# Performance work log

Hardware: AMD Instinct MI355X
Metric: run time of the kernel (lower is better)

## Reference

```python
import jax, jax.numpy as jnp
import numpy as np
from jax.ops import segment_sum

N_NODES = 100000
N_EDGES = 1600000
HIDDEN = 64
N_LAYERS = 4
N_CLASSES = 10
N_GRAPHS = 512


def setup_inputs() -> dict:
    key = jax.random.key(0)
    ks = jax.random.split(key, 9)
    x = jax.random.normal(ks[0], (N_NODES, HIDDEN), dtype=jnp.float32)
    edge_index = jax.random.randint(ks[1], (2, N_EDGES), 0, N_NODES, dtype=jnp.int32)
    batch = jnp.sort(jax.random.randint(ks[2], (N_NODES,), 0, N_GRAPHS, dtype=jnp.int32))
    s = 0.05
    W_enc = jax.random.normal(ks[3], (HIDDEN, HIDDEN), dtype=jnp.float32) * s
    b_enc = jax.random.normal(ks[4], (HIDDEN,), dtype=jnp.float32) * s
    W_conv = jax.random.normal(ks[5], (N_LAYERS, HIDDEN, HIDDEN), dtype=jnp.float32) * s
    b_conv = jax.random.normal(ks[6], (N_LAYERS, HIDDEN), dtype=jnp.float32) * s
    W_out = jax.random.normal(ks[7], (HIDDEN, N_CLASSES), dtype=jnp.float32) * s
    b_out = jax.random.normal(ks[8], (N_CLASSES,), dtype=jnp.float32) * s
    return {"x": x, "edge_index": edge_index, "batch": batch,
            "W_enc": W_enc, "b_enc": b_enc, "W_conv": W_conv, "b_conv": b_conv,
            "W_out": W_out, "b_out": b_out, "num_graphs": N_GRAPHS}


def reference(x, edge_index, batch, W_enc, b_enc, W_conv, b_conv, W_out, b_out, num_graphs):
    N = x.shape[0]
    src, dst = edge_index[0], edge_index[1]
    # atom_encoder: Linear
    h = x @ W_enc + b_enc
    # GCN symmetric normalization with self-loops (PyG GCNConv default):
    # deg counts incoming edges (dst) plus the self-loop.
    deg = segment_sum(jnp.ones_like(src, dtype=h.dtype), dst, num_segments=N) + 1.0
    deg_inv_sqrt = jax.lax.rsqrt(deg)
    deg_inv = 1.0 / deg  # self-loop norm = d^-1/2 * d^-1/2
    edge_norm = (deg_inv_sqrt[src] * deg_inv_sqrt[dst])[:, None]  # [E,1]
    for l in range(W_conv.shape[0]):
        hl = h @ W_conv[l]                          # [N,H]
        msg = hl[src] * edge_norm                   # gather + normalize [E,H]
        agg = segment_sum(msg, dst, num_segments=N) # scatter-add
        h = agg + hl * deg_inv[:, None] + b_conv[l] # self-loop + bias
        h = jax.nn.silu(h)                          # dropout p=0 / eval: identity
    # global_add_pool over graph ids
    pooled = segment_sum(h, batch, num_segments=num_graphs)  # [G,H]
    # readout: Linear + ReLU (make_mlp with hidden_layers=1)
    out = jax.nn.relu(pooled @ W_out + b_out)
    return out
```

## Files before the change

kernel.cpp:

```cpp
#include <hip/hip_runtime.h>
#include <math.h>

#define HIDDEN 64
#define N_LAYERS 4
#define N_CLASSES 10
#define N_GRAPHS 512
#define BSH 8
#define NPB 256
#define PART_K 2048

typedef _Float16 __h;
typedef __attribute__((ext_vector_type(4))) _Float16 half4;
typedef __attribute__((ext_vector_type(8))) _Float16 half8;
typedef __attribute__((ext_vector_type(4))) float f32x4;

__global__ __launch_bounds__(256) void k_histA(const int* __restrict__ dst,
                                               int* __restrict__ ghist, int E, int NB) {
    __shared__ int hist[512];
    int t = threadIdx.x;
    hist[t] = 0; hist[t + 256] = 0;
    __syncthreads();
    int base = blockIdx.x * PART_K;
    int kend = min(PART_K, E - base);
    for (int k = t; k < kend; k += 256) atomicAdd(&hist[dst[base + k] >> BSH], 1);
    __syncthreads();
    for (int j = t; j < NB; j += 256) {
        int h = hist[j];
        if (h) atomicAdd(&ghist[j], h);
    }
}

__global__ __launch_bounds__(256) void k_bucketscan(const int* __restrict__ ghist,
                                                    int* __restrict__ bucketbase,
                                                    int* __restrict__ gcur, int NB) {
    __shared__ int s[256];
    int t = threadIdx.x;
    int j0 = 2 * t, j1 = 2 * t + 1;
    int h0 = (j0 < NB) ? ghist[j0] : 0;
    int h1 = (j1 < NB) ? ghist[j1] : 0;
    s[t] = h0 + h1; __syncthreads();
    for (int o = 1; o < 256; o <<= 1) {
        int x = (t >= o) ? s[t - o] : 0;
        __syncthreads();
        s[t] += x;
        __syncthreads();
    }
    int base = (t == 0) ? 0 : s[t - 1];
    if (j0 <= NB) { bucketbase[j0] = base;      gcur[j0] = base; }
    if (j1 <= NB) { bucketbase[j1] = base + h0; gcur[j1] = base + h0; }
}

__global__ __launch_bounds__(256) void k_partition(const int* __restrict__ src,
                                                   const int* __restrict__ dst,
                                                   int* __restrict__ gcur,
                                                   int* __restrict__ packed,
                                                   int E, int NB) {
    __shared__ int hist[512];
    __shared__ int scanE[512];
    __shared__ int cur[512];
    __shared__ int delta[512];
    __shared__ int ps[256];
    __shared__ int stage[PART_K];
    __shared__ unsigned short stgj[PART_K];
    int t = threadIdx.x;
    int base = blockIdx.x * PART_K;
    int kend = min(PART_K, E - base);

    hist[t] = 0; hist[t + 256] = 0;
    __syncthreads();
    for (int k = t; k < kend; k += 256) atomicAdd(&hist[dst[base + k] >> BSH], 1);
    __syncthreads();

    int j0 = 2 * t, j1 = j0 + 1;
    int h0 = hist[j0], h1 = hist[j1];
    ps[t] = h0 + h1; __syncthreads();
    for (int o = 1; o < 256; o <<= 1) {
        int x = (t >= o) ? ps[t - o] : 0;
        __syncthreads();
        ps[t] += x;
        __syncthreads();
    }
    int bexc = (t == 0) ? 0 : ps[t - 1];
    scanE[j0] = bexc;
    scanE[j1] = bexc + h0;
    __syncthreads();

    for (int j = t; j < NB; j += 256) {
        int h = hist[j];
        int g = h ? atomicAdd(&gcur[j], h) : 0;
        delta[j] = g - scanE[j];
        cur[j]   = scanE[j];
    }
    __syncthreads();

    for (int k = t; k < kend; k += 256) {
        int d = dst[base + k], s = src[base + k];
        int j = d >> BSH;
        int pos = atomicAdd(&cur[j], 1);
        stage[pos] = (s << BSH) | (d & (NPB - 1));
        stgj[pos]  = (unsigned short)j;
    }
    __syncthreads();

    for (int i = t; i < kend; i += 256) {
        packed[i + delta[stgj[i]]] = stage[i];
    }
}

__global__ __launch_bounds__(256) void k_fill3(const int* __restrict__ packed,
                                               const int* __restrict__ bucketbase,
                                               int* __restrict__ rowptr,
                                               float* __restrict__ dis,
                                               int* __restrict__ csr_src,
                                               int N, int E) {
    __shared__ int cnt[256];
    __shared__ int rp[256];
    int j = blockIdx.x;
    int t = threadIdx.x;
    int node0 = j << BSH;
    int segb = bucketbase[j];
    int sege = bucketbase[j + 1];

    cnt[t] = 0; __syncthreads();
    for (int i = segb + t; i < sege; i += 256) atomicAdd(&cnt[packed[i] & (NPB - 1)], 1);
    __syncthreads();

    int c = cnt[t];
    rp[t] = c; __syncthreads();
    for (int o = 1; o < 256; o <<= 1) {
        int x = (t >= o) ? rp[t - o] : 0;
        __syncthreads();
        rp[t] += x;
        __syncthreads();
    }
    int node = node0 + t;
    int start = segb + rp[t] - c + node;
    if (node < N) {
        rowptr[node] = start;
        dis[node] = rsqrtf((float)c + 1.0f);
        csr_src[start] = node;
        if (node == N - 1) rowptr[N] = E + N;
    }
    __syncthreads();
    cnt[t] = start + 1;
    __syncthreads();
    for (int i = segb + t; i < sege; i += 256) {
        int v = packed[i];
        int slot = atomicAdd(&cnt[v & (NPB - 1)], 1);
        csr_src[slot] = v >> BSH;
    }
}

__device__ __forceinline__ half4 shfl_xor_h4(half4 v, int m) {
    uint2 u = __builtin_bit_cast(uint2, v);
    u.x = __shfl_xor((int)u.x, m);
    u.y = __shfl_xor((int)u.y, m);
    return __builtin_bit_cast(half4, u);
}

__global__ __launch_bounds__(256) void k_prepW(const float* __restrict__ Wconv,
                                               const float* __restrict__ Wenc,
                                               __h* __restrict__ Wh) {
    int idx = blockIdx.x * 256 + threadIdx.x;
    int l = idx >> 12;
    int kn = idx & 4095;
    int k = kn >> 6, n = kn & 63;
    int nt = n >> 4, nl = n & 15;
    int kt = k >> 5, kr = k & 31;
    int quad = kr >> 3, j = kr & 7;
    int lane = quad * 16 + nl;
    int pos = (((nt * 2 + kt) * 64 + lane) << 3) + j;
    float w = (l < N_LAYERS) ? Wconv[(size_t)l * 4096 + kn] : Wenc[kn];
    Wh[(l << 12) + pos] = (__h)w;
}

__global__ __launch_bounds__(256) void k_layer(const int* __restrict__ csr_src,
                                               const int* __restrict__ rowptr,
                                               const float* __restrict__ dis,
                                               const __h* __restrict__ G,
                                               const __h* __restrict__ Wh,
                                               const float* __restrict__ bias,
                                               const int* __restrict__ batch,
                                               __h* __restrict__ Gho,
                                               float* __restrict__ pooled,
                                               int N, int last) {
    __shared__ __attribute__((aligned(16))) __h At[4][16][72];
    int wave = threadIdx.x >> 6;
    int lane = threadIdx.x & 63;
    int row0 = (blockIdx.x * 4 + wave) * 16;
    if (row0 >= N) return;
    int grp = lane >> 4;
    int f4  = lane & 15;

    int rpi = row0 + lane;
    int rpv = rowptr[rpi > N ? N : rpi];

    const half4 z = {(__h)0.f, (__h)0.f, (__h)0.f, (__h)0.f};
    for (int i = 0; i < 16; ++i) {
        int beg = __shfl(rpv, i);
        int end = __shfl(rpv, i + 1);
        half4 a = z;
        int e = beg + grp;
        while (e < end) {
            int s0 = csr_src[e];
            int s1 = (e + 4  < end) ? csr_src[e + 4]  : -1;
            int s2 = (e + 8  < end) ? csr_src[e + 8]  : -1;
            int s3 = (e + 12 < end) ? csr_src[e + 12] : -1;
            int s4 = (e + 16 < end) ? csr_src[e + 16] : -1;
            int s5 = (e + 20 < end) ? csr_src[e + 20] : -1;
            int s6 = (e + 24 < end) ? csr_src[e + 24] : -1;
            int s7 = (e + 28 < end) ? csr_src[e + 28] : -1;
            half4 r0 = ((const half4*)(G + (size_t)s0 * 64))[f4];
            half4 r1 = (s1 >= 0) ? ((const half4*)(G + (size_t)s1 * 64))[f4] : z;
            half4 r2 = (s2 >= 0) ? ((const half4*)(G + (size_t)s2 * 64))[f4] : z;
            half4 r3 = (s3 >= 0) ? ((const half4*)(G + (size_t)s3 * 64))[f4] : z;
            half4 r4 = (s4 >= 0) ? ((const half4*)(G + (size_t)s4 * 64))[f4] : z;
            half4 r5 = (s5 >= 0) ? ((const half4*)(G + (size_t)s5 * 64))[f4] : z;
            half4 r6 = (s6 >= 0) ? ((const half4*)(G + (size_t)s6 * 64))[f4] : z;
            half4 r7 = (s7 >= 0) ? ((const half4*)(G + (size_t)s7 * 64))[f4] : z;
            a += r0; a += r1; a += r2; a += r3;
            a += r4; a += r5; a += r6; a += r7;
            e += 32;
        }
        a += shfl_xor_h4(a, 16);
        a += shfl_xor_h4(a, 32);
        if (grp == 0) {
            int node = row0 + i;
            float df = (node < N) ? dis[node] : 0.0f;
            __h dd = (__h)df;
            ((half4*)&At[wave][i][0])[f4] = a * dd;
        }
    }

    int quad = grp, nl = f4;
    half8 bf[4][2];
    #pragma unroll
    for (int nt = 0; nt < 4; ++nt)
        #pragma unroll
        for (int kt = 0; kt < 2; ++kt)
            bf[nt][kt] = *(const half8*)(Wh + (((nt * 2 + kt) * 64 + lane) << 3));

    half8 a0 = *(const half8*)&At[wave][nl][quad * 8];
    half8 a1 = *(const half8*)&At[wave][nl][32 + quad * 8];

    f32x4 acc[4];
    #pragma unroll
    for (int nt = 0; nt < 4; ++nt) {
        acc[nt] = (f32x4){0.f, 0.f, 0.f, 0.f};
        acc[nt] = __builtin_amdgcn_mfma_f32_16x16x32_f16(a0, bf[nt][0], acc[nt], 0, 0, 0);
        acc[nt] = __builtin_amdgcn_mfma_f32_16x16x32_f16(a1, bf[nt][1], acc[nt], 0, 0, 0);
    }

    float b[4];
    #pragma unroll
    for (int nt = 0; nt < 4; ++nt) b[nt] = bias[nt * 16 + nl];

    if (!last) {
        #pragma unroll
        for (int reg = 0; reg < 4; ++reg) {
            int rr = row0 + quad * 4 + reg;
            if (rr < N) {
                float ds_ = dis[rr];
                #pragma unroll
                for (int nt = 0; nt < 4; ++nt) {
                    float v = acc[nt][reg] + b[nt];
                    v = v / (1.0f + expf(-v));
                    Gho[(size_t)rr * 64 + nt * 16 + nl] = (__h)(ds_ * v);
                }
            }
        }
    } else {
        float run[4] = {0.f, 0.f, 0.f, 0.f};
        int cur = -1;
        #pragma unroll
        for (int reg = 0; reg < 4; ++reg) {
            int rr = row0 + quad * 4 + reg;
            if (rr < N) {
                int bi = batch[rr];
                float vals[4];
                #pragma unroll
                for (int nt = 0; nt < 4; ++nt) {
                    float v = acc[nt][reg] + b[nt];
                    vals[nt] = v / (1.0f + expf(-v));
                }
                if (bi != cur) {
                    if (cur >= 0) {
                        #pragma unroll
                        for (int nt = 0; nt < 4; ++nt)
                            atomicAdd(&pooled[cur * 64 + nt * 16 + nl], run[nt]);
                    }
                    cur = bi;
                    #pragma unroll
                    for (int nt = 0; nt < 4; ++nt) run[nt] = vals[nt];
                } else {
                    #pragma unroll
                    for (int nt = 0; nt < 4; ++nt) run[nt] += vals[nt];
                }
            }
        }
        if (cur >= 0) {
            #pragma unroll
            for (int nt = 0; nt < 4; ++nt)
                atomicAdd(&pooled[cur * 64 + nt * 16 + nl], run[nt]);
        }
    }
}

__global__ __launch_bounds__(256) void k_gemm_mfma(const float* __restrict__ xf,
                                                   const __h* __restrict__ Wh,
                                                   const float* __restrict__ bias,
                                                   const float* __restrict__ dis,
                                                   __h* __restrict__ Gho,
                                                   int N) {
    int wave = threadIdx.x >> 6;
    int lane = threadIdx.x & 63;
    int row0 = (blockIdx.x * 4 + wave) * 32;
    if (row0 >= N) return;
    int quad = lane >> 4, nl = lane & 15;

    half8 bf[4][2];
    #pragma unroll
    for (int nt = 0; nt < 4; ++nt)
        #pragma unroll
        for (int kt = 0; kt < 2; ++kt)
            bf[nt][kt] = *(const half8*)(Wh + (((nt * 2 + kt) * 64 + lane) << 3));

    f32x4 acc[2][4];
    #pragma unroll
    for (int h = 0; h < 2; ++h) {
        int r = row0 + h * 16 + nl; if (r >= N) r = N - 1;
        const float* ap = xf + (size_t)r * 64 + quad * 8;
        float4 v0 = ((const float4*)ap)[0];
        float4 v1 = ((const float4*)ap)[1];
        float4 v2 = ((const float4*)(ap + 32))[0];
        float4 v3 = ((const float4*)(ap + 32))[1];
        half8 a0 = (half8){(__h)v0.x, (__h)v0.y, (__h)v0.z, (__h)v0.w,
                           (__h)v1.x, (__h)v1.y, (__h)v1.z, (__h)v1.w};
        half8 a1 = (half8){(__h)v2.x, (__h)v2.y, (__h)v2.z, (__h)v2.w,
                           (__h)v3.x, (__h)v3.y, (__h)v3.z, (__h)v3.w};
        #pragma unroll
        for (int nt = 0; nt < 4; ++nt) {
            acc[h][nt] = (f32x4){0.f, 0.f, 0.f, 0.f};
            acc[h][nt] = __builtin_amdgcn_mfma_f32_16x16x32_f16(a0, bf[nt][0], acc[h][nt], 0, 0, 0);
            acc[h][nt] = __builtin_amdgcn_mfma_f32_16x16x32_f16(a1, bf[nt][1], acc[h][nt], 0, 0, 0);
        }
    }

    float b[4];
    #pragma unroll
    for (int nt = 0; nt < 4; ++nt) b[nt] = bias[nt * 16 + nl];

    #pragma unroll
    for (int h = 0; h < 2; ++h) {
        #pragma unroll
        for (int reg = 0; reg < 4; ++reg) {
            int rr = row0 + h * 16 + quad * 4 + reg;
            if (rr < N) {
                float ds = dis[rr];
                #pragma unroll
                for (int nt = 0; nt < 4; ++nt) {
                    float v = acc[h][nt][reg] + b[nt];
                    Gho[(size_t)rr * 64 + nt * 16 + nl] = (__h)(ds * v);
                }
            }
        }
    }
}

__global__ __launch_bounds__(256) void k_readout(const float* __restrict__ pooled,
                                                 const float* __restrict__ Wout,
                                                 const float* __restrict__ bout,
                                                 float* __restrict__ out) {
    int idx = blockIdx.x * 256 + threadIdx.x;
    if (idx >= N_GRAPHS * N_CLASSES) return;
    int g = idx / N_CLASSES, c = idx % N_CLASSES;
    float s = bout[c];
    #pragma unroll
    for (int j = 0; j < 64; ++j) s += pooled[g * 64 + j] * Wout[j * N_CLASSES + c];
    out[idx] = fmaxf(s, 0.0f);
}

extern "C" void kernel_launch(void* const* d_in, const int* in_sizes, int n_in,
                              void* d_out, int out_size, void* d_ws, size_t ws_size,
                              hipStream_t stream) {
    const float* x      = (const float*)d_in[0];
    const int*   ei     = (const int*)d_in[1];
    const int*   batch  = (const int*)d_in[2];
    const float* W_enc  = (const float*)d_in[3];
    const float* b_enc  = (const float*)d_in[4];
    const float* W_conv = (const float*)d_in[5];
    const float* b_conv = (const float*)d_in[6];
    const float* W_out  = (const float*)d_in[7];
    const float* b_out  = (const float*)d_in[8];
    float* out = (float*)d_out;

    const int N = in_sizes[2];
    const int E = in_sizes[1] / 2;
    const int* src = ei;
    const int* dst = ei + E;
    const int NB   = (N + NPB - 1) >> BSH;
    const int NBLK = (E + PART_K - 1) / PART_K;

    char* ws = (char*)d_ws;
    size_t off = 0;
    auto alloc = [&](size_t bytes) -> char* {
        char* p = ws + off;
        off += (bytes + 255) & ~(size_t)255;
        return p;
    };
    int*   ghist      = (int*)alloc((size_t)(NB + 1) * sizeof(int));
    int*   bucketbase = (int*)alloc((size_t)(NB + 1) * sizeof(int));
    int*   gcur       = (int*)alloc((size_t)(NB + 1) * sizeof(int));
    int*   packed     = (int*)alloc((size_t)E * sizeof(int));
    int*   csr_src    = (int*)alloc((size_t)(E + N) * sizeof(int));
    int*   rowptr     = (int*)alloc((size_t)(N + 1) * sizeof(int));
    float* dis        = (float*)alloc((size_t)N * sizeof(float));
    __h*   bufA       = (__h*)alloc((size_t)N * HIDDEN * sizeof(__h));
    __h*   bufB       = (__h*)alloc((size_t)N * HIDDEN * sizeof(__h));
    __h*   Wh         = (__h*)alloc((size_t)(N_LAYERS + 1) * 4096 * sizeof(__h));
    float* pooled     = (float*)alloc((size_t)N_GRAPHS * HIDDEN * sizeof(float));
    (void)ws_size;

    hipMemsetAsync(ghist, 0, (size_t)(NB + 1) * sizeof(int), stream);
    hipMemsetAsync(pooled, 0, (size_t)N_GRAPHS * HIDDEN * sizeof(float), stream);

    k_histA     <<<NBLK, 256, 0, stream>>>(dst, ghist, E, NB);
    k_bucketscan<<<1,    256, 0, stream>>>(ghist, bucketbase, gcur, NB);
    k_partition <<<NBLK, 256, 0, stream>>>(src, dst, gcur, packed, E, NB);
    k_fill3     <<<NB,   256, 0, stream>>>(packed, bucketbase, rowptr, dis, csr_src, N, E);
    k_prepW<<<((N_LAYERS + 1) * 4096) / 256, 256, 0, stream>>>(W_conv, W_enc, Wh);

    int gb32 = (N + 127) / 128;
    k_gemm_mfma<<<gb32, 256, 0, stream>>>(x, Wh + (size_t)N_LAYERS * 4096, b_enc,
                                          dis, bufA, N);

    __h* bufs[2] = {bufA, bufB};
    int glayer = (N + 63) / 64;
    for (int l = 0; l < N_LAYERS; ++l) {
        int last = (l == N_LAYERS - 1);
        k_layer<<<glayer, 256, 0, stream>>>(csr_src, rowptr, dis, bufs[l & 1],
                                            Wh + (size_t)l * 4096,
                                            b_conv + (size_t)l * HIDDEN, batch,
                                            bufs[(l + 1) & 1], pooled, N, last);
    }

    k_readout<<<(N_GRAPHS * N_CLASSES + 255) / 256, 256, 0, stream>>>(pooled, W_out, b_out, out);
}
```

Baseline: 336.8 us.

## Split each 16-row tile across two waves and stage CSR indices in LDS

The layer kernel now gives each 16-row tile to two waves, each aggregating 8 rows, so a block covers 32 rows and twice as many blocks are launched. The tile's CSR source indices are loaded cooperatively and coalesced into shared memory before the gather, with a fallback to global memory past a 512-entry cap. Both waves compute the MFMA redundantly and each writes back only its half. The aim is more parallelism on the latency-bound gather and cheaper index loads, at the cost of two block barriers, duplicated MFMA work and extra shared memory.

```diff
diff --git a/kernel.cpp b/kernel.cpp
--- a/kernel.cpp
+++ b/kernel.cpp
@@ -8,6 +8,7 @@
 #define BSH 8
 #define NPB 256
 #define PART_K 2048
+#define IDX_CAP 512
 
 typedef _Float16 __h;
 typedef __attribute__((ext_vector_type(4))) _Float16 half4;
@@ -184,32 +185,47 @@
                                                __h* __restrict__ Gho,
                                                float* __restrict__ pooled,
                                                int N, int last) {
-    __shared__ __attribute__((aligned(16))) __h At[4][16][72];
-    int wave = threadIdx.x >> 6;
-    int lane = threadIdx.x & 63;
-    int row0 = (blockIdx.x * 4 + wave) * 16;
-    if (row0 >= N) return;
+    __shared__ __attribute__((aligned(16))) __h At[2][16][72];
+    __shared__ int sidx[2][IDX_CAP];
+    int tid  = threadIdx.x;
+    int wave = tid >> 6;
+    int lane = tid & 63;
+    int tile = wave >> 1;
+    int half = wave & 1;
+    int trow0 = blockIdx.x * 32 + tile * 16;
     int grp = lane >> 4;
     int f4  = lane & 15;
 
-    int rpi = row0 + lane;
+    int rpi = trow0 + lane;
     int rpv = rowptr[rpi > N ? N : rpi];
+    int beg0 = __shfl(rpv, 0);
+    int endL = __shfl(rpv, 16);
+    int Lc   = endL - beg0; if (Lc > IDX_CAP) Lc = IDX_CAP;
+
+    int t2 = tid & 127;
+    const int* __restrict__ gsrc = csr_src + beg0;
+    for (int k = t2; k < Lc; k += 128) sidx[tile][k] = gsrc[k];
+    __syncthreads();
 
     const half4 z = {(__h)0.f, (__h)0.f, (__h)0.f, (__h)0.f};
-    for (int i = 0; i < 16; ++i) {
+    const int* sp = sidx[tile];
+    #pragma unroll 2
+    for (int r = 0; r < 8; ++r) {
+        int i = half * 8 + r;
         int beg = __shfl(rpv, i);
         int end = __shfl(rpv, i + 1);
         half4 a = z;
         int e = beg + grp;
         while (e < end) {
-            int s0 = csr_src[e];
-            int s1 = (e + 4  < end) ? csr_src[e + 4]  : -1;
-            int s2 = (e + 8  < end) ? csr_src[e + 8]  : -1;
-            int s3 = (e + 12 < end) ? csr_src[e + 12] : -1;
-            int s4 = (e + 16 < end) ? csr_src[e + 16] : -1;
-            int s5 = (e + 20 < end) ? csr_src[e + 20] : -1;
-            int s6 = (e + 24 < end) ? csr_src[e + 24] : -1;
-            int s7 = (e + 28 < end) ? csr_src[e + 28] : -1;
+            int o = e - beg0;
+            int s0 =                  (o      < IDX_CAP) ? sp[o]      : csr_src[e];
+            int s1 = (e + 4  < end) ? ((o + 4  < IDX_CAP) ? sp[o + 4]  : csr_src[e + 4])  : -1;
+            int s2 = (e + 8  < end) ? ((o + 8  < IDX_CAP) ? sp[o + 8]  : csr_src[e + 8])  : -1;
+            int s3 = (e + 12 < end) ? ((o + 12 < IDX_CAP) ? sp[o + 12] : csr_src[e + 12]) : -1;
+            int s4 = (e + 16 < end) ? ((o + 16 < IDX_CAP) ? sp[o + 16] : csr_src[e + 16]) : -1;
+            int s5 = (e + 20 < end) ? ((o + 20 < IDX_CAP) ? sp[o + 20] : csr_src[e + 20]) : -1;
+            int s6 = (e + 24 < end) ? ((o + 24 < IDX_CAP) ? sp[o + 24] : csr_src[e + 24]) : -1;
+            int s7 = (e + 28 < end) ? ((o + 28 < IDX_CAP) ? sp[o + 28] : csr_src[e + 28]) : -1;
             half4 r0 = ((const half4*)(G + (size_t)s0 * 64))[f4];
             half4 r1 = (s1 >= 0) ? ((const half4*)(G + (size_t)s1 * 64))[f4] : z;
             half4 r2 = (s2 >= 0) ? ((const half4*)(G + (size_t)s2 * 64))[f4] : z;
@@ -225,12 +241,13 @@
         a += shfl_xor_h4(a, 16);
         a += shfl_xor_h4(a, 32);
         if (grp == 0) {
-            int node = row0 + i;
+            int node = trow0 + i;
             float df = (node < N) ? dis[node] : 0.0f;
             __h dd = (__h)df;
-            ((half4*)&At[wave][i][0])[f4] = a * dd;
-        }
-    }
+            ((half4*)&At[tile][i][0])[f4] = a * dd;
+        }
+    }
+    __syncthreads();
 
     int quad = grp, nl = f4;
     half8 bf[4][2];
@@ -240,8 +257,8 @@
         for (int kt = 0; kt < 2; ++kt)
             bf[nt][kt] = *(const half8*)(Wh + (((nt * 2 + kt) * 64 + lane) << 3));
 
-    half8 a0 = *(const half8*)&At[wave][nl][quad * 8];
-    half8 a1 = *(const half8*)&At[wave][nl][32 + quad * 8];
+    half8 a0 = *(const half8*)&At[tile][nl][quad * 8];
+    half8 a1 = *(const half8*)&At[tile][nl][32 + quad * 8];
 
     f32x4 acc[4];
     #pragma unroll
@@ -255,53 +272,59 @@
     #pragma unroll
     for (int nt = 0; nt < 4; ++nt) b[nt] = bias[nt * 16 + nl];
 
+    bool own = ((quad >> 1) == half);
+
     if (!last) {
-        #pragma unroll
-        for (int reg = 0; reg < 4; ++reg) {
-            int rr = row0 + quad * 4 + reg;
-            if (rr < N) {
-                float ds_ = dis[rr];
-                #pragma unroll
-                for (int nt = 0; nt < 4; ++nt) {
-                    float v = acc[nt][reg] + b[nt];
-                    v = v / (1.0f + expf(-v));
-                    Gho[(size_t)rr * 64 + nt * 16 + nl] = (__h)(ds_ * v);
+        if (own) {
+            #pragma unroll
+            for (int reg = 0; reg < 4; ++reg) {
+                int rr = trow0 + quad * 4 + reg;
+                if (rr < N) {
+                    float ds_ = dis[rr];
+                    #pragma unroll
+                    for (int nt = 0; nt < 4; ++nt) {
+                        float v = acc[nt][reg] + b[nt];
+                        v = v / (1.0f + expf(-v));
+                        Gho[(size_t)rr * 64 + nt * 16 + nl] = (__h)(ds_ * v);
+                    }
                 }
             }
         }
     } else {
-        float run[4] = {0.f, 0.f, 0.f, 0.f};
-        int cur = -1;
-        #pragma unroll
-        for (int reg = 0; reg < 4; ++reg) {
-            int rr = row0 + quad * 4 + reg;
-            if (rr < N) {
-                int bi = batch[rr];
-                float vals[4];
-                #pragma unroll
-                for (int nt = 0; nt < 4; ++nt) {
-                    float v = acc[nt][reg] + b[nt];
-                    vals[nt] = v / (1.0f + expf(-v));
-                }
-                if (bi != cur) {
-                    if (cur >= 0) {
+        if (own) {
+            float run[4] = {0.f, 0.f, 0.f, 0.f};
+            int cur = -1;
+            #pragma unroll
+            for (int reg = 0; reg < 4; ++reg) {
+                int rr = trow0 + quad * 4 + reg;
+                if (rr < N) {
+                    int bi = batch[rr];
+                    float vals[4];
+                    #pragma unroll
+                    for (int nt = 0; nt < 4; ++nt) {
+                        float v = acc[nt][reg] + b[nt];
+                        vals[nt] = v / (1.0f + expf(-v));
+                    }
+                    if (bi != cur) {
+                        if (cur >= 0) {
+                            #pragma unroll
+                            for (int nt = 0; nt < 4; ++nt)
+                                atomicAdd(&pooled[cur * 64 + nt * 16 + nl], run[nt]);
+                        }
+                        cur = bi;
                         #pragma unroll
-                        for (int nt = 0; nt < 4; ++nt)
-                            atomicAdd(&pooled[cur * 64 + nt * 16 + nl], run[nt]);
+                        for (int nt = 0; nt < 4; ++nt) run[nt] = vals[nt];
+                    } else {
+                        #pragma unroll
+                        for (int nt = 0; nt < 4; ++nt) run[nt] += vals[nt];
                     }
-                    cur = bi;
-                    #pragma unroll
-                    for (int nt = 0; nt < 4; ++nt) run[nt] = vals[nt];
-                } else {
-                    #pragma unroll
-                    for (int nt = 0; nt < 4; ++nt) run[nt] += vals[nt];
                 }
             }
-        }
-        if (cur >= 0) {
-            #pragma unroll
-            for (int nt = 0; nt < 4; ++nt)
-                atomicAdd(&pooled[cur * 64 + nt * 16 + nl], run[nt]);
+            if (cur >= 0) {
+                #pragma unroll
+                for (int nt = 0; nt < 4; ++nt)
+                    atomicAdd(&pooled[cur * 64 + nt * 16 + nl], run[nt]);
+            }
         }
     }
 }
@@ -435,7 +458,7 @@
                                           dis, bufA, N);
 
     __h* bufs[2] = {bufA, bufB};
-    int glayer = (N + 63) / 64;
+    int glayer = (N + 31) / 32;
     for (int l = 0; l < N_LAYERS; ++l) {
         int last = (l == N_LAYERS - 1);
         k_layer<<<glayer, 256, 0, stream>>>(csr_src, rowptr, dis, bufs[l & 1],
```

Result: slower. 349.1 us (+3.6%).
